# Optimization experiments

Hardware: AMD Instinct MI355X
Metric: run time of the kernel (lower is better)

The kernel has to match this reference:

```python
import jax, jax.numpy as jnp
import numpy as np


def setup_inputs() -> dict:
    key = jax.random.key(0)
    ks = jax.random.split(key, 7)
    B, T, Fin, H, O = 32, 2048, 256, 256, 256
    s = 1.0 / np.sqrt(H)
    return {
        "x":   jax.random.normal(ks[0], (B, T, Fin), dtype=jnp.float32),
        "h0":  jax.random.normal(ks[1], (B, H), dtype=jnp.float32),
        "Wxh": jax.random.normal(ks[2], (H, Fin), dtype=jnp.float32) * s,
        "bxh": jax.random.normal(ks[3], (H,), dtype=jnp.float32) * s,
        "Whh": jax.random.normal(ks[4], (H, H), dtype=jnp.float32) * s,
        "Why": jax.random.normal(ks[5], (O, H), dtype=jnp.float32) * s,
        "by":  jax.random.normal(ks[6], (O,), dtype=jnp.float32) * s,
    }


def reference(x, h0, Wxh, bxh, Whh, Why, by):
    # Batch the input projection across all T as one GEMM: (B,T,Fin)x(Fin,H)
    xh = jnp.einsum('btf,hf->bth', x, Wxh) + bxh  # (B,T,H)

    def step(h, xh_t):
        h = jnp.tanh(xh_t + h @ Whh.T)  # (B,H)
        return h, h

    # scan over time (axis 0 after transpose)
    h_final, hs = jax.lax.scan(step, h0, jnp.swapaxes(xh, 0, 1))  # hs: (T,B,H)
    hs = jnp.swapaxes(hs, 0, 1)  # (B,T,H)
    # Batch the output projection across all T as one GEMM
    y = jnp.einsum('bth,oh->bto', hs, Why) + by  # (B,T,O)
    return (y, h_final)
```

## Files before the change

### kernel.cpp

```cpp
#include <hip/hip_runtime.h>
#include <hip/hip_fp16.h>


typedef _Float16 f16x8 __attribute__((ext_vector_type(8)));
typedef float    f32x4 __attribute__((ext_vector_type(4)));

#define MFMA16 __builtin_amdgcn_mfma_f32_16x16x32_f16

__device__ __forceinline__ f16x8 cvt8(const float* __restrict__ p) {
    float4 u = *(const float4*)p;
    float4 v = *(const float4*)(p + 4);
    f16x8 r;
    r[0] = (_Float16)u.x; r[1] = (_Float16)u.y; r[2] = (_Float16)u.z; r[3] = (_Float16)u.w;
    r[4] = (_Float16)v.x; r[5] = (_Float16)v.y; r[6] = (_Float16)v.z; r[7] = (_Float16)v.w;
    return r;
}

template<bool AF16, bool OF16>
__global__ __launch_bounds__(512, 2) void gemm_nt_512(
    const void* __restrict__ Av, const float* __restrict__ W,
    const float* __restrict__ bias, void* __restrict__ Cv) {
    const int tid = threadIdx.x;
    const int l  = tid & 63;
    const int w  = tid >> 6;
    const int lr = l & 15;
    const int lg = l >> 4;
    const long m0 = (long)blockIdx.x * 128;
    const int  n0 = w * 32;

    f16x8 wg[2][8];
    #pragma unroll
    for (int nt = 0; nt < 2; ++nt)
        #pragma unroll
        for (int k = 0; k < 8; ++k)
            wg[nt][k] = cvt8(W + (long)(n0 + nt * 16 + lr) * 256 + k * 32 + lg * 8);

    const float bv0 = bias[n0 + lr];
    const float bv1 = bias[n0 + 16 + lr];

    #pragma unroll 2
    for (int mt = 0; mt < 8; ++mt) {
        const long r0 = m0 + mt * 16 + lr;
        f32x4 ac[2] = {{0.f,0.f,0.f,0.f},{0.f,0.f,0.f,0.f}};
        #pragma unroll
        for (int k = 0; k < 8; ++k) {
            const int kc = k * 32 + lg * 8;
            f16x8 a;
            if constexpr (AF16) a = *(const f16x8*)((const _Float16*)Av + r0 * 256 + kc);
            else                a = cvt8((const float*)Av + r0 * 256 + kc);
            ac[0] = MFMA16(a, wg[0][k], ac[0], 0, 0, 0);
            ac[1] = MFMA16(a, wg[1][k], ac[1], 0, 0, 0);
        }
        #pragma unroll
        for (int nt = 0; nt < 2; ++nt) {
            const int col = n0 + nt * 16 + lr;
            const float bv = nt ? bv1 : bv0;
            #pragma unroll
            for (int d = 0; d < 4; ++d) {
                const long row = m0 + mt * 16 + lg * 4 + d;
                const float v = ac[nt][d] + bv;
                if constexpr (OF16) ((_Float16*)Cv)[row * 256 + col] = (_Float16)v;
                else                ((float*)Cv)[row * 256 + col] = v;
            }
        }
    }
}

__global__ __launch_bounds__(512, 1) void rnn_scan(
    const _Float16* __restrict__ xh, const float* __restrict__ h0,
    const float* __restrict__ Whh, _Float16* __restrict__ hs,
    float* __restrict__ hfin) {
    const int b   = blockIdx.x;
    const int tid = threadIdx.x;
    const int l   = tid & 63;
    const int w   = tid >> 6;
    const int lr  = l & 15;
    const int lg  = l >> 4;
    const int n0  = w * 32;

    __shared__ _Float16 hbuf[2][256];

    f16x8 wb[2][8];
    #pragma unroll
    for (int nt = 0; nt < 2; ++nt)
        #pragma unroll
        for (int k = 0; k < 8; ++k)
            wb[nt][k] = cvt8(Whh + (long)(n0 + nt * 16 + lr) * 256 + k * 32 + lg * 8);

    if (tid < 256) hbuf[0][tid] = (_Float16)h0[b * 256 + tid];
    __syncthreads();

    const int cl = n0 + (l & 31);
    const _Float16* xp = xh + (long)b * 2048 * 256 + cl;
    _Float16*       hp = hs + (long)b * 2048 * 256 + cl;

    float xcur[4], xnext[4];
    #pragma unroll
    for (int j = 0; j < 4; ++j) xcur[j] = (float)xp[(long)j * 256];

    for (int tb = 0; tb < 2048; tb += 4) {
        #pragma unroll
        for (int j = 0; j < 4; ++j) {
            long tn = tb + 4 + j; if (tn > 2047) tn = 2047;
            xnext[j] = (float)xp[tn * 256];
        }

        #pragma unroll
        for (int j = 0; j < 4; ++j) {
            const f16x8* hc = (const f16x8*)hbuf[j & 1];
            f16x8 af[8];
            #pragma unroll
            for (int k = 0; k < 8; ++k) af[k] = hc[k * 4 + lg];

            __builtin_amdgcn_s_setprio(1);
            const f32x4 zero = {0.f, 0.f, 0.f, 0.f};
            f32x4 accA[2], accB[2];
            #pragma unroll
            for (int nt = 0; nt < 2; ++nt) {
                accA[nt] = MFMA16(af[0], wb[nt][0], zero, 0, 0, 0);
                accB[nt] = MFMA16(af[4], wb[nt][4], zero, 0, 0, 0);
            }
            #pragma unroll
            for (int k = 1; k < 4; ++k)
                #pragma unroll
                for (int nt = 0; nt < 2; ++nt) {
                    accA[nt] = MFMA16(af[k],     wb[nt][k],     accA[nt], 0, 0, 0);
                    accB[nt] = MFMA16(af[k + 4], wb[nt][k + 4], accB[nt], 0, 0, 0);
                }
            __builtin_amdgcn_s_setprio(0);

            const float s0 = accA[0][0] + accB[0][0];
            const float s1 = accA[1][0] + accB[1][0];
            const float s  = ((l & 16) ? s1 : s0) + xcur[j];
            const float e  = __expf(2.0f * s);
            const float v  = 1.0f - 2.0f * __builtin_amdgcn_rcpf(e + 1.0f);
            const _Float16 hv = (_Float16)v;

            if (l < 32) {
                hbuf[(j & 1) ^ 1][cl] = hv;
                hp[(long)(tb + j) * 256] = hv;
            }

            asm volatile("s_waitcnt lgkmcnt(0)" ::: "memory");
            __builtin_amdgcn_s_barrier();
            asm volatile("" ::: "memory");
        }

        #pragma unroll
        for (int j = 0; j < 4; ++j) xcur[j] = xnext[j];
    }

    if (tid < 256) hfin[b * 256 + tid] = (float)hbuf[0][tid];
}

extern "C" void kernel_launch(void* const* d_in, const int* in_sizes, int n_in,
                              void* d_out, int out_size, void* d_ws, size_t ws_size,
                              hipStream_t stream) {
    const float* x   = (const float*)d_in[0];
    const float* h0  = (const float*)d_in[1];
    const float* Wxh = (const float*)d_in[2];
    const float* bxh = (const float*)d_in[3];
    const float* Whh = (const float*)d_in[4];
    const float* Why = (const float*)d_in[5];
    const float* by  = (const float*)d_in[6];

    float* y    = (float*)d_out;
    float* hfin = y + (long)65536 * 256;
    _Float16* xhf = (_Float16*)(y + (long)32768 * 256);
    _Float16* hs  = (_Float16*)d_ws;

    gemm_nt_512<false, true ><<<512, 512, 0, stream>>>(x, Wxh, bxh, xhf);
    rnn_scan<<<32, 512, 0, stream>>>(xhf, h0, Whh, hs, hfin);
    gemm_nt_512<true,  false><<<512, 512, 0, stream>>>(hs, Why, by, y);
}
```

Before: 920.2 us.

## Fuse input projection, recurrent scan and output projection into one kernel

Merges the two projection GEMMs and the recurrent scan into a single per-batch kernel, so each of the 32 blocks computes its own input projection, runs the scan, then computes its own output projection. This removes two kernel launches and the inter-kernel boundaries. The trade-off is that both GEMMs now run on only 32 workgroups instead of 512, which sharply reduces the parallelism available to them.

```diff
diff --git a/kernel.cpp b/kernel.cpp
--- a/kernel.cpp
+++ b/kernel.cpp
@@ -16,60 +16,14 @@
     return r;
 }
 
-template<bool AF16, bool OF16>
-__global__ __launch_bounds__(512, 2) void gemm_nt_512(
-    const void* __restrict__ Av, const float* __restrict__ W,
-    const float* __restrict__ bias, void* __restrict__ Cv) {
-    const int tid = threadIdx.x;
-    const int l  = tid & 63;
-    const int w  = tid >> 6;
-    const int lr = l & 15;
-    const int lg = l >> 4;
-    const long m0 = (long)blockIdx.x * 128;
-    const int  n0 = w * 32;
-
-    f16x8 wg[2][8];
-    #pragma unroll
-    for (int nt = 0; nt < 2; ++nt)
-        #pragma unroll
-        for (int k = 0; k < 8; ++k)
-            wg[nt][k] = cvt8(W + (long)(n0 + nt * 16 + lr) * 256 + k * 32 + lg * 8);
-
-    const float bv0 = bias[n0 + lr];
-    const float bv1 = bias[n0 + 16 + lr];
-
-    #pragma unroll 2
-    for (int mt = 0; mt < 8; ++mt) {
-        const long r0 = m0 + mt * 16 + lr;
-        f32x4 ac[2] = {{0.f,0.f,0.f,0.f},{0.f,0.f,0.f,0.f}};
-        #pragma unroll
-        for (int k = 0; k < 8; ++k) {
-            const int kc = k * 32 + lg * 8;
-            f16x8 a;
-            if constexpr (AF16) a = *(const f16x8*)((const _Float16*)Av + r0 * 256 + kc);
-            else                a = cvt8((const float*)Av + r0 * 256 + kc);
-            ac[0] = MFMA16(a, wg[0][k], ac[0], 0, 0, 0);
-            ac[1] = MFMA16(a, wg[1][k], ac[1], 0, 0, 0);
-        }
-        #pragma unroll
-        for (int nt = 0; nt < 2; ++nt) {
-            const int col = n0 + nt * 16 + lr;
-            const float bv = nt ? bv1 : bv0;
-            #pragma unroll
-            for (int d = 0; d < 4; ++d) {
-                const long row = m0 + mt * 16 + lg * 4 + d;
-                const float v = ac[nt][d] + bv;
-                if constexpr (OF16) ((_Float16*)Cv)[row * 256 + col] = (_Float16)v;
-                else                ((float*)Cv)[row * 256 + col] = v;
-            }
-        }
-    }
-}
-
-__global__ __launch_bounds__(512, 1) void rnn_scan(
-    const _Float16* __restrict__ xh, const float* __restrict__ h0,
-    const float* __restrict__ Whh, _Float16* __restrict__ hs,
-    float* __restrict__ hfin) {
+__global__ __launch_bounds__(512, 1) void rnn_fused(
+    const float* __restrict__ x,   const float* __restrict__ h0,
+    const float* __restrict__ Wxh, const float* __restrict__ bxh,
+    const float* __restrict__ Whh, const float* __restrict__ Why,
+    const float* __restrict__ by,
+    float* __restrict__ y,
+    float* __restrict__ hfin,
+    _Float16* __restrict__ hs) {
     const int b   = blockIdx.x;
     const int tid = threadIdx.x;
     const int l   = tid & 63;
@@ -77,80 +31,152 @@
     const int lr  = l & 15;
     const int lg  = l >> 4;
     const int n0  = w * 32;
+    const int cl  = n0 + (l & 31);
 
     __shared__ _Float16 hbuf[2][256];
 
-    f16x8 wb[2][8];
-    #pragma unroll
-    for (int nt = 0; nt < 2; ++nt)
+    const float* xb  = x  + (long)b * 2048 * 256;
+    float*       yb  = y  + (long)b * 2048 * 256;
+    _Float16*    hpB = hs + (long)b * 2048 * 256;
+    _Float16*    xhf = (_Float16*)(yb + (long)1024 * 256);
+
+    {
+        f16x8 wgx[2][8];
         #pragma unroll
-        for (int k = 0; k < 8; ++k)
-            wb[nt][k] = cvt8(Whh + (long)(n0 + nt * 16 + lr) * 256 + k * 32 + lg * 8);
+        for (int nt = 0; nt < 2; ++nt)
+            #pragma unroll
+            for (int k = 0; k < 8; ++k)
+                wgx[nt][k] = cvt8(Wxh + (long)(n0 + nt * 16 + lr) * 256 + k * 32 + lg * 8);
+        const float bv0 = bxh[n0 + lr];
+        const float bv1 = bxh[n0 + 16 + lr];
+
+        #pragma unroll 2
+        for (int mt = 0; mt < 128; ++mt) {
+            f32x4 ac[2] = {{0.f,0.f,0.f,0.f},{0.f,0.f,0.f,0.f}};
+            #pragma unroll
+            for (int k = 0; k < 8; ++k) {
+                const int kc = k * 32 + lg * 8;
+                f16x8 a = cvt8(xb + (long)(mt * 16 + lr) * 256 + kc);
+                ac[0] = MFMA16(a, wgx[0][k], ac[0], 0, 0, 0);
+                ac[1] = MFMA16(a, wgx[1][k], ac[1], 0, 0, 0);
+            }
+            #pragma unroll
+            for (int nt = 0; nt < 2; ++nt) {
+                const int col = n0 + nt * 16 + lr;
+                const float bv = nt ? bv1 : bv0;
+                #pragma unroll
+                for (int d = 0; d < 4; ++d)
+                    xhf[(long)(mt * 16 + lg * 4 + d) * 256 + col] =
+                        (_Float16)(ac[nt][d] + bv);
+            }
+        }
+    }
 
     if (tid < 256) hbuf[0][tid] = (_Float16)h0[b * 256 + tid];
     __syncthreads();
 
-    const int cl = n0 + (l & 31);
-    const _Float16* xp = xh + (long)b * 2048 * 256 + cl;
-    _Float16*       hp = hs + (long)b * 2048 * 256 + cl;
+    {
+        f16x8 wb[2][8];
+        #pragma unroll
+        for (int nt = 0; nt < 2; ++nt)
+            #pragma unroll
+            for (int k = 0; k < 8; ++k)
+                wb[nt][k] = cvt8(Whh + (long)(n0 + nt * 16 + lr) * 256 + k * 32 + lg * 8);
 
-    float xcur[4], xnext[4];
-    #pragma unroll
-    for (int j = 0; j < 4; ++j) xcur[j] = (float)xp[(long)j * 256];
+        const _Float16* xp = xhf + cl;
+        _Float16*       hp = hpB + cl;
 
-    for (int tb = 0; tb < 2048; tb += 4) {
+        float xcur[4], xnext[4];
         #pragma unroll
-        for (int j = 0; j < 4; ++j) {
-            long tn = tb + 4 + j; if (tn > 2047) tn = 2047;
-            xnext[j] = (float)xp[tn * 256];
+        for (int j = 0; j < 4; ++j) xcur[j] = (float)xp[(long)j * 256];
+
+        for (int tb = 0; tb < 2048; tb += 4) {
+            #pragma unroll
+            for (int j = 0; j < 4; ++j) {
+                long tn = tb + 4 + j; if (tn > 2047) tn = 2047;
+                xnext[j] = (float)xp[tn * 256];
+            }
+
+            #pragma unroll
+            for (int j = 0; j < 4; ++j) {
+                const f16x8* hc = (const f16x8*)hbuf[j & 1];
+                f16x8 af[8];
+                #pragma unroll
+                for (int k = 0; k < 8; ++k) af[k] = hc[k * 4 + lg];
+
+                __builtin_amdgcn_s_setprio(1);
+                const f32x4 zero = {0.f, 0.f, 0.f, 0.f};
+                f32x4 accA[2], accB[2];
+                #pragma unroll
+                for (int nt = 0; nt < 2; ++nt) {
+                    accA[nt] = MFMA16(af[0], wb[nt][0], zero, 0, 0, 0);
+                    accB[nt] = MFMA16(af[4], wb[nt][4], zero, 0, 0, 0);
+                }
+                #pragma unroll
+                for (int k = 1; k < 4; ++k)
+                    #pragma unroll
+                    for (int nt = 0; nt < 2; ++nt) {
+                        accA[nt] = MFMA16(af[k],     wb[nt][k],     accA[nt], 0, 0, 0);
+                        accB[nt] = MFMA16(af[k + 4], wb[nt][k + 4], accB[nt], 0, 0, 0);
+                    }
+                __builtin_amdgcn_s_setprio(0);
+
+                const float s0 = accA[0][0] + accB[0][0];
+                const float s1 = accA[1][0] + accB[1][0];
+                const float s  = ((l & 16) ? s1 : s0) + xcur[j];
+                const float e  = __expf(2.0f * s);
+                const float v  = 1.0f - 2.0f * __builtin_amdgcn_rcpf(e + 1.0f);
+                const _Float16 hv = (_Float16)v;
+
+                if (l < 32) {
+                    hbuf[(j & 1) ^ 1][cl] = hv;
+                    hp[(long)(tb + j) * 256] = hv;
+                }
+
+                asm volatile("s_waitcnt lgkmcnt(0)" ::: "memory");
+                __builtin_amdgcn_s_barrier();
+                asm volatile("" ::: "memory");
+            }
+
+            #pragma unroll
+            for (int j = 0; j < 4; ++j) xcur[j] = xnext[j];
         }
 
+        if (tid < 256) hfin[b * 256 + tid] = (float)hbuf[0][tid];
+    }
+
+    __syncthreads();
+
+    {
+        f16x8 wgy[2][8];
         #pragma unroll
-        for (int j = 0; j < 4; ++j) {
-            const f16x8* hc = (const f16x8*)hbuf[j & 1];
-            f16x8 af[8];
+        for (int nt = 0; nt < 2; ++nt)
             #pragma unroll
-            for (int k = 0; k < 8; ++k) af[k] = hc[k * 4 + lg];
+            for (int k = 0; k < 8; ++k)
+                wgy[nt][k] = cvt8(Why + (long)(n0 + nt * 16 + lr) * 256 + k * 32 + lg * 8);
+        const float bv0 = by[n0 + lr];
+        const float bv1 = by[n0 + 16 + lr];
 
-            __builtin_amdgcn_s_setprio(1);
-            const f32x4 zero = {0.f, 0.f, 0.f, 0.f};
-            f32x4 accA[2], accB[2];
+        #pragma unroll 2
+        for (int mt = 0; mt < 128; ++mt) {
+            f32x4 ac[2] = {{0.f,0.f,0.f,0.f},{0.f,0.f,0.f,0.f}};
+            #pragma unroll
+            for (int k = 0; k < 8; ++k) {
+                const int kc = k * 32 + lg * 8;
+                f16x8 a = *(const f16x8*)(hpB + (long)(mt * 16 + lr) * 256 + kc);
+                ac[0] = MFMA16(a, wgy[0][k], ac[0], 0, 0, 0);
+                ac[1] = MFMA16(a, wgy[1][k], ac[1], 0, 0, 0);
+            }
             #pragma unroll
             for (int nt = 0; nt < 2; ++nt) {
-                accA[nt] = MFMA16(af[0], wb[nt][0], zero, 0, 0, 0);
-                accB[nt] = MFMA16(af[4], wb[nt][4], zero, 0, 0, 0);
+                const int col = n0 + nt * 16 + lr;
+                const float bv = nt ? bv1 : bv0;
+                #pragma unroll
+                for (int d = 0; d < 4; ++d)
+                    yb[(long)(mt * 16 + lg * 4 + d) * 256 + col] = ac[nt][d] + bv;
             }
-            #pragma unroll
-            for (int k = 1; k < 4; ++k)
-                #pragma unroll
-                for (int nt = 0; nt < 2; ++nt) {
-                    accA[nt] = MFMA16(af[k],     wb[nt][k],     accA[nt], 0, 0, 0);
-                    accB[nt] = MFMA16(af[k + 4], wb[nt][k + 4], accB[nt], 0, 0, 0);
-                }
-            __builtin_amdgcn_s_setprio(0);
-
-            const float s0 = accA[0][0] + accB[0][0];
-            const float s1 = accA[1][0] + accB[1][0];
-            const float s  = ((l & 16) ? s1 : s0) + xcur[j];
-            const float e  = __expf(2.0f * s);
-            const float v  = 1.0f - 2.0f * __builtin_amdgcn_rcpf(e + 1.0f);
-            const _Float16 hv = (_Float16)v;
-
-            if (l < 32) {
-                hbuf[(j & 1) ^ 1][cl] = hv;
-                hp[(long)(tb + j) * 256] = hv;
-            }
-
-            asm volatile("s_waitcnt lgkmcnt(0)" ::: "memory");
-            __builtin_amdgcn_s_barrier();
-            asm volatile("" ::: "memory");
         }
-
-        #pragma unroll
-        for (int j = 0; j < 4; ++j) xcur[j] = xnext[j];
     }
-
-    if (tid < 256) hfin[b * 256 + tid] = (float)hbuf[0][tid];
 }
 
 extern "C" void kernel_launch(void* const* d_in, const int* in_sizes, int n_in,
@@ -166,10 +192,7 @@
 
     float* y    = (float*)d_out;
     float* hfin = y + (long)65536 * 256;
-    _Float16* xhf = (_Float16*)(y + (long)32768 * 256);
-    _Float16* hs  = (_Float16*)d_ws;
+    _Float16* hs = (_Float16*)d_ws;
 
-    gemm_nt_512<false, true ><<<512, 512, 0, stream>>>(x, Wxh, bxh, xhf);
-    rnn_scan<<<32, 512, 0, stream>>>(xhf, h0, Whh, hs, hfin);
-    gemm_nt_512<true,  false><<<512, 512, 0, stream>>>(hs, Why, by, y);
+    rnn_fused<<<32, 512, 0, stream>>>(x, h0, Wxh, bxh, Whh, Why, by, y, hfin, hs);
 }
```

After: 1.549 ms. 1.68x slower.

## Fuse input GEMM, scan and output GEMM into one flag-synchronized persistent kernel

Applied to the files above, without the earlier changes.

Merges the three launches into one kernel where blocks 0-31 run the recurrent scan, blocks 32-63 compute output projections as hs chunks become ready, and the rest compute the input projection per 128-step chunk. Ready chunks are signalled through global acquire/release flags. This lets the GEMMs overlap with the latency-bound serial scan instead of running before and after it. It relies on all spinning blocks being co-resident to avoid deadlock, and it adds spin-wait and fence overhead inside the scan loop.

```diff
diff --git a/kernel.cpp b/kernel.cpp
--- a/kernel.cpp
+++ b/kernel.cpp
@@ -6,6 +6,9 @@
 typedef float    f32x4 __attribute__((ext_vector_type(4)));
 
 #define MFMA16 __builtin_amdgcn_mfma_f32_16x16x32_f16
+#define AQ  __ATOMIC_ACQUIRE
+#define RL  __ATOMIC_RELEASE
+#define AGT __HIP_MEMORY_SCOPE_AGENT
 
 __device__ __forceinline__ f16x8 cvt8(const float* __restrict__ p) {
     float4 u = *(const float4*)p;
@@ -17,16 +20,14 @@
 }
 
 template<bool AF16, bool OF16>
-__global__ __launch_bounds__(512, 2) void gemm_nt_512(
-    const void* __restrict__ Av, const float* __restrict__ W,
-    const float* __restrict__ bias, void* __restrict__ Cv) {
-    const int tid = threadIdx.x;
+__device__ __forceinline__ void gemm128(
+    const void* __restrict__ Ap, const float* __restrict__ W,
+    const float* __restrict__ bias, void* __restrict__ Cp, int tid) {
     const int l  = tid & 63;
     const int w  = tid >> 6;
     const int lr = l & 15;
     const int lg = l >> 4;
-    const long m0 = (long)blockIdx.x * 128;
-    const int  n0 = w * 32;
+    const int n0 = w * 32;
 
     f16x8 wg[2][8];
     #pragma unroll
@@ -34,20 +35,20 @@
         #pragma unroll
         for (int k = 0; k < 8; ++k)
             wg[nt][k] = cvt8(W + (long)(n0 + nt * 16 + lr) * 256 + k * 32 + lg * 8);
-
     const float bv0 = bias[n0 + lr];
     const float bv1 = bias[n0 + 16 + lr];
 
     #pragma unroll 2
     for (int mt = 0; mt < 8; ++mt) {
-        const long r0 = m0 + mt * 16 + lr;
         f32x4 ac[2] = {{0.f,0.f,0.f,0.f},{0.f,0.f,0.f,0.f}};
         #pragma unroll
         for (int k = 0; k < 8; ++k) {
             const int kc = k * 32 + lg * 8;
             f16x8 a;
-            if constexpr (AF16) a = *(const f16x8*)((const _Float16*)Av + r0 * 256 + kc);
-            else                a = cvt8((const float*)Av + r0 * 256 + kc);
+            if constexpr (AF16)
+                a = *(const f16x8*)((const _Float16*)Ap + (long)(mt * 16 + lr) * 256 + kc);
+            else
+                a = cvt8((const float*)Ap + (long)(mt * 16 + lr) * 256 + kc);
             ac[0] = MFMA16(a, wg[0][k], ac[0], 0, 0, 0);
             ac[1] = MFMA16(a, wg[1][k], ac[1], 0, 0, 0);
         }
@@ -57,26 +58,63 @@
             const float bv = nt ? bv1 : bv0;
             #pragma unroll
             for (int d = 0; d < 4; ++d) {
-                const long row = m0 + mt * 16 + lg * 4 + d;
+                const long row = mt * 16 + lg * 4 + d;
                 const float v = ac[nt][d] + bv;
-                if constexpr (OF16) ((_Float16*)Cv)[row * 256 + col] = (_Float16)v;
-                else                ((float*)Cv)[row * 256 + col] = v;
-            }
-        }
-    }
-}
-
-__global__ __launch_bounds__(512, 1) void rnn_scan(
-    const _Float16* __restrict__ xh, const float* __restrict__ h0,
-    const float* __restrict__ Whh, _Float16* __restrict__ hs,
-    float* __restrict__ hfin) {
+                if constexpr (OF16) ((_Float16*)Cp)[row * 256 + col] = (_Float16)v;
+                else                ((float*)Cp)[row * 256 + col] = v;
+            }
+        }
+    }
+}
+
+__global__ __launch_bounds__(512, 1) void rnn_all(
+    const float* __restrict__ x,   const float* __restrict__ h0,
+    const float* __restrict__ Wxh, const float* __restrict__ bxh,
+    const float* __restrict__ Whh, const float* __restrict__ Why,
+    const float* __restrict__ by,
+    float* __restrict__ y,
+    float* __restrict__ hfin,
+    _Float16* __restrict__ hs,
+    int* __restrict__ xhflag,
+    int* __restrict__ hsflag) {
+    const int tid = threadIdx.x;
+    _Float16* xhf = (_Float16*)(y + (long)32768 * 256);
+
+    if (blockIdx.x >= 64) {
+        const int idx = blockIdx.x - 64;
+        const int mc  = idx >> 5;
+        const int b   = idx & 31;
+        const long off = ((long)b * 2048 + mc * 128) * 256;
+        gemm128<false, true>(x + off, Wxh, bxh, xhf + off, tid);
+        __threadfence();
+        __syncthreads();
+        if (tid == 0) __hip_atomic_store(&xhflag[idx], 1, RL, AGT);
+        return;
+    }
+
+    if (blockIdx.x >= 32) {
+        const int c = blockIdx.x - 32;
+        for (int k = 0; k < 16; ++k) {
+            while (!__hip_atomic_load(&hsflag[c * 16 + k], AQ, AGT))
+                __builtin_amdgcn_s_sleep(2);
+            if (c >= 16) {
+                const int b0 = 2 * (c - 16) + (k >> 3);
+                while (!__hip_atomic_load(&hsflag[b0 * 16 + 2 * (k & 7) + 1], AQ, AGT))
+                    __builtin_amdgcn_s_sleep(2);
+            }
+            const long off = ((long)c * 2048 + k * 128) * 256;
+            gemm128<true, false>(hs + off, Why, by, y + off, tid);
+        }
+        return;
+    }
+
     const int b   = blockIdx.x;
-    const int tid = threadIdx.x;
     const int l   = tid & 63;
     const int w   = tid >> 6;
     const int lr  = l & 15;
     const int lg  = l >> 4;
     const int n0  = w * 32;
+    const int cl  = n0 + (l & 31);
 
     __shared__ _Float16 hbuf[2][256];
 
@@ -90,15 +128,25 @@
     if (tid < 256) hbuf[0][tid] = (_Float16)h0[b * 256 + tid];
     __syncthreads();
 
-    const int cl = n0 + (l & 31);
-    const _Float16* xp = xh + (long)b * 2048 * 256 + cl;
-    _Float16*       hp = hs + (long)b * 2048 * 256 + cl;
+    while (!__hip_atomic_load(&xhflag[0 * 32 + b], AQ, AGT))
+        __builtin_amdgcn_s_sleep(2);
+
+    const _Float16* xp = xhf + (long)b * 2048 * 256 + cl;
+    _Float16*       hp = hs  + (long)b * 2048 * 256 + cl;
 
     float xcur[4], xnext[4];
     #pragma unroll
     for (int j = 0; j < 4; ++j) xcur[j] = (float)xp[(long)j * 256];
 
+    int acqd = 0;
     for (int tb = 0; tb < 2048; tb += 4) {
+        const int need = (tb + 7) >> 7;
+        if (need > acqd) {
+            while (!__hip_atomic_load(&xhflag[need * 32 + b], AQ, AGT))
+                __builtin_amdgcn_s_sleep(2);
+            acqd = need;
+        }
+
         #pragma unroll
         for (int j = 0; j < 4; ++j) {
             long tn = tb + 4 + j; if (tn > 2047) tn = 2047;
@@ -144,6 +192,13 @@
             asm volatile("s_waitcnt lgkmcnt(0)" ::: "memory");
             __builtin_amdgcn_s_barrier();
             asm volatile("" ::: "memory");
+        }
+
+        if (((tb + 4) & 127) == 0) {
+            __threadfence();
+            __syncthreads();
+            if (tid == 0)
+                __hip_atomic_store(&hsflag[b * 16 + ((tb + 4) >> 7) - 1], 1, RL, AGT);
         }
 
         #pragma unroll
@@ -166,10 +221,11 @@
 
     float* y    = (float*)d_out;
     float* hfin = y + (long)65536 * 256;
-    _Float16* xhf = (_Float16*)(y + (long)32768 * 256);
-    _Float16* hs  = (_Float16*)d_ws;
-
-    gemm_nt_512<false, true ><<<512, 512, 0, stream>>>(x, Wxh, bxh, xhf);
-    rnn_scan<<<32, 512, 0, stream>>>(xhf, h0, Whh, hs, hfin);
-    gemm_nt_512<true,  false><<<512, 512, 0, stream>>>(hs, Why, by, y);
-}
+    _Float16* hs = (_Float16*)d_ws;
+    int* xhflag = (int*)((char*)d_ws + 33554432);
+    int* hsflag = xhflag + 512;
+
+    hipMemsetAsync(xhflag, 0, 4096, stream);
+    rnn_all<<<576, 512, 0, stream>>>(x, h0, Wxh, bxh, Whh, Why, by,
+                                     y, hfin, hs, xhflag, hsflag);
+}
```

Result: slower. 1.335 ms (+45.1%).
